# Kernel tuning notes

Measured on AMD Instinct MI355X. Metric: run time of the kernel, lower is better.

Reference implementation:

```python
import jax, jax.numpy as jnp
import numpy as np

B, N, C = 32, 16384, 256
D, H, S = 64, 128, 7
ITERS = 3
EPS = 1e-6
SCALE = D ** -0.5


def _ln(x, g, b):
    m = jnp.mean(x, axis=-1, keepdims=True)
    v = jnp.var(x, axis=-1, keepdims=True)
    return (x - m) / jnp.sqrt(v + 1e-5) * g + b


def _gru(x, h, Wih, Whh, bih, bhh):
    # PyTorch GRUCell: Wih/Whh are [3D, D]
    gi = x @ Wih.T + bih
    gh = h @ Whh.T + bhh
    ir, iz, inn = jnp.split(gi, 3, axis=-1)
    hr, hz, hn = jnp.split(gh, 3, axis=-1)
    r = jax.nn.sigmoid(ir + hr)
    z = jax.nn.sigmoid(iz + hz)
    n = jnp.tanh(inn + r * hn)
    return (1.0 - z) * n + z * h


def setup_inputs() -> dict:
    key = jax.random.key(0)
    ks = jax.random.split(key, 20)
    s_c = C ** -0.5
    s_d = D ** -0.5
    s_h = H ** -0.5
    p = {}
    p["inputs"] = jax.random.normal(ks[0], (B, N, C), jnp.float32)
    p["slots_mu"] = jax.random.normal(ks[1], (B, S, D), jnp.float32)
    p["ln_in_g"] = jnp.ones((C,), jnp.float32)
    p["ln_in_b"] = jnp.zeros((C,), jnp.float32)
    p["Wk"] = jax.random.normal(ks[2], (C, D), jnp.float32) * s_c
    p["Wv"] = jax.random.normal(ks[3], (C, D), jnp.float32) * s_c
    p["q_ln_g"] = jnp.ones((D,), jnp.float32)
    p["q_ln_b"] = jnp.zeros((D,), jnp.float32)
    p["Wq"] = jax.random.normal(ks[4], (D, D), jnp.float32) * s_d
    p["bq_ln_g"] = jnp.ones((D,), jnp.float32)
    p["bq_ln_b"] = jnp.zeros((D,), jnp.float32)
    p["bWq"] = jax.random.normal(ks[5], (D, D), jnp.float32) * s_d
    p["gru_Wih"] = jax.random.normal(ks[6], (3 * D, D), jnp.float32) * s_d
    p["gru_Whh"] = jax.random.normal(ks[7], (3 * D, D), jnp.float32) * s_d
    p["gru_bih"] = jnp.zeros((3 * D,), jnp.float32)
    p["gru_bhh"] = jnp.zeros((3 * D,), jnp.float32)
    p["mlp_ln_g"] = jnp.ones((D,), jnp.float32)
    p["mlp_ln_b"] = jnp.zeros((D,), jnp.float32)
    p["mlp_W1"] = jax.random.normal(ks[8], (D, H), jnp.float32) * s_d
    p["mlp_b1"] = jnp.zeros((H,), jnp.float32)
    p["mlp_W2"] = jax.random.normal(ks[9], (H, D), jnp.float32) * s_h
    p["mlp_b2"] = jnp.zeros((D,), jnp.float32)
    p["bmlp_ln_g"] = jnp.ones((D,), jnp.float32)
    p["bmlp_ln_b"] = jnp.zeros((D,), jnp.float32)
    p["bmlp_W1"] = jax.random.normal(ks[10], (D, H), jnp.float32) * s_d
    p["bmlp_b1"] = jnp.zeros((H,), jnp.float32)
    p["bmlp_W2"] = jax.random.normal(ks[11], (H, D), jnp.float32) * s_h
    p["bmlp_b2"] = jnp.zeros((D,), jnp.float32)
    return p


def reference(inputs, slots_mu, ln_in_g, ln_in_b, Wk, Wv, q_ln_g, q_ln_b, Wq,
              bq_ln_g, bq_ln_b, bWq, gru_Wih, gru_Whh, gru_bih, gru_bhh,
              mlp_ln_g, mlp_ln_b, mlp_W1, mlp_b1, mlp_W2, mlp_b2,
              bmlp_ln_g, bmlp_ln_b, bmlp_W1, bmlp_b1, bmlp_W2, bmlp_b2):
    x = _ln(inputs, ln_in_g, ln_in_b)          # [B,N,C]
    k = x @ Wk                                  # [B,N,D]
    v = x @ Wv                                  # [B,N,D]
    fg = slots_mu[:, :-1]                       # [B,S-1,D]
    bg = slots_mu[:, -1:]                       # [B,1,D]
    for _ in range(ITERS):
        fg_prev, bg_prev = fg, bg
        fq = _ln(fg, q_ln_g, q_ln_b) @ Wq
        bq = _ln(bg, bq_ln_g, bq_ln_b) @ bWq
        q = jnp.concatenate([fq, bq], axis=1)   # [B,S,D]
        logits = SCALE * jnp.einsum('bnd,bmd->bnm', k, q)  # [B,N,S]
        attn = jax.nn.softmax(logits, axis=-1) + EPS
        fa = attn[..., :-1]
        ba = attn[..., -1:]
        fa = fa / jnp.sum(fa, axis=1, keepdims=True)
        ba = ba / jnp.sum(ba, axis=1, keepdims=True)
        fu = jnp.einsum('bnm,bnd->bmd', fa, v)  # [B,S-1,D]
        bu = jnp.einsum('bnm,bnd->bmd', ba, v)  # [B,1,D]
        fg = _gru(fu.reshape(-1, D), fg_prev.reshape(-1, D),
                  gru_Wih, gru_Whh, gru_bih, gru_bhh).reshape(B, S - 1, D)
        fg = fg + (jax.nn.relu(_ln(fg, mlp_ln_g, mlp_ln_b) @ mlp_W1 + mlp_b1) @ mlp_W2 + mlp_b2)
        # NOTE: original code uses self.gru (shared) for bg, not bg_gru
        bg = _gru(bu.reshape(-1, D), bg_prev.reshape(-1, D),
                  gru_Wih, gru_Whh, gru_bih, gru_bhh).reshape(B, 1, D)
        bg = bg + (jax.nn.relu(_ln(bg, bmlp_ln_g, bmlp_ln_b) @ bmlp_W1 + bmlp_b1) @ bmlp_W2 + bmlp_b2)
    return jnp.concatenate([fg, bg], axis=1)    # [B,S,D]
```

## Files before the change

kernel.cpp:

```cpp
#include <hip/hip_runtime.h>
#include <hip/hip_bf16.h>

typedef __bf16 bf16_t;
typedef __bf16 bf16x4 __attribute__((ext_vector_type(4)));
typedef __bf16 bf16x8 __attribute__((ext_vector_type(8)));
typedef float f32x4 __attribute__((ext_vector_type(4)));

#define B_ 32
#define N_ 16384
#define C_ 256
#define D_ 64
#define ROWS_TOTAL (B_ * N_)

__device__ inline float wave_sum64(float v) {
#pragma unroll
  for (int o = 1; o < 64; o <<= 1) v += __shfl_xor(v, o);
  return v;
}

__device__ inline float sigmoidf_(float x) { return 1.0f / (1.0f + __expf(-x)); }
__device__ inline float tanhf_(float x) { return 1.0f - 2.0f / (__expf(2.0f * x) + 1.0f); }

__global__ __launch_bounds__(256) void prep_kernel(
    const float* __restrict__ Wk, const float* __restrict__ Wv,
    const float* __restrict__ Wih, const float* __restrict__ Whh,
    const float* __restrict__ slots, bf16_t* __restrict__ Wb,
    float* __restrict__ WihT, float* __restrict__ WhhT, float* __restrict__ g) {
  int i = blockIdx.x * 256 + threadIdx.x;
  if (i < 32768) {
    int j = i & 7, l = (i >> 3) & 63, t = (i >> 9) & 7, kb = i >> 12;
    int k = kb * 32 + (l >> 4) * 8 + j;
    int n = t * 16 + (l & 15);
    float v = (n < 64) ? Wk[k * 64 + n] : Wv[k * 64 + (n - 64)];
    Wb[i] = (bf16_t)v;
  } else if (i < 45056) {
    int idx = i - 32768;
    int c = idx / 192, j = idx % 192;
    WihT[idx] = Wih[j * 64 + c];
  } else if (i < 57344) {
    int idx = i - 45056;
    int c = idx / 192, j = idx % 192;
    WhhT[idx] = Whh[j * 64 + c];
  } else if (i < 71680) {
    int idx = i - 57344;
    g[idx] = slots[idx];
  }
}

__global__ __launch_bounds__(512) void proj_ln_kernel(
    const float* __restrict__ inp, const float* __restrict__ lng,
    const float* __restrict__ lnb, const bf16_t* __restrict__ Wb,
    bf16_t* __restrict__ kbuf, bf16_t* __restrict__ vbuf) {
  __shared__ bf16_t xs[128 * 256];
  const int tid = threadIdx.x, w = tid >> 6, lane = tid & 63;
  const int q4 = lane >> 4, lp = lane & 15;
  const long row0 = (long)blockIdx.x * 128;

  float4 gv[4], bv[4];
#pragma unroll
  for (int j = 0; j < 4; ++j) {
    gv[j] = *(const float4*)(lng + lp * 16 + j * 4);
    bv[j] = *(const float4*)(lnb + lp * 16 + j * 4);
  }

#pragma unroll
  for (int i = 0; i < 4; ++i) {
    int r = w * 16 + i * 4 + q4;
    const float* rp = inp + (row0 + r) * C_ + lp * 16;
    float4 x0 = *(const float4*)(rp);
    float4 x1 = *(const float4*)(rp + 4);
    float4 x2 = *(const float4*)(rp + 8);
    float4 x3 = *(const float4*)(rp + 12);
    float s = (x0.x + x0.y + x0.z + x0.w) + (x1.x + x1.y + x1.z + x1.w) +
              (x2.x + x2.y + x2.z + x2.w) + (x3.x + x3.y + x3.z + x3.w);
    float s2 = (x0.x * x0.x + x0.y * x0.y + x0.z * x0.z + x0.w * x0.w) +
               (x1.x * x1.x + x1.y * x1.y + x1.z * x1.z + x1.w * x1.w) +
               (x2.x * x2.x + x2.y * x2.y + x2.z * x2.z + x2.w * x2.w) +
               (x3.x * x3.x + x3.y * x3.y + x3.z * x3.z + x3.w * x3.w);
#pragma unroll
    for (int o = 1; o < 16; o <<= 1) {
      s += __shfl_xor(s, o);
      s2 += __shfl_xor(s2, o);
    }
    float mean = s * (1.0f / 256.0f);
    float var = s2 * (1.0f / 256.0f) - mean * mean;
    float rstd = rsqrtf(var + 1e-5f);
    bf16x8 y0, y1;
    y0[0] = (bf16_t)((x0.x - mean) * rstd * gv[0].x + bv[0].x);
    y0[1] = (bf16_t)((x0.y - mean) * rstd * gv[0].y + bv[0].y);
    y0[2] = (bf16_t)((x0.z - mean) * rstd * gv[0].z + bv[0].z);
    y0[3] = (bf16_t)((x0.w - mean) * rstd * gv[0].w + bv[0].w);
    y0[4] = (bf16_t)((x1.x - mean) * rstd * gv[1].x + bv[1].x);
    y0[5] = (bf16_t)((x1.y - mean) * rstd * gv[1].y + bv[1].y);
    y0[6] = (bf16_t)((x1.z - mean) * rstd * gv[1].z + bv[1].z);
    y0[7] = (bf16_t)((x1.w - mean) * rstd * gv[1].w + bv[1].w);
    y1[0] = (bf16_t)((x2.x - mean) * rstd * gv[2].x + bv[2].x);
    y1[1] = (bf16_t)((x2.y - mean) * rstd * gv[2].y + bv[2].y);
    y1[2] = (bf16_t)((x2.z - mean) * rstd * gv[2].z + bv[2].z);
    y1[3] = (bf16_t)((x2.w - mean) * rstd * gv[2].w + bv[2].w);
    y1[4] = (bf16_t)((x3.x - mean) * rstd * gv[3].x + bv[3].x);
    y1[5] = (bf16_t)((x3.y - mean) * rstd * gv[3].y + bv[3].y);
    y1[6] = (bf16_t)((x3.z - mean) * rstd * gv[3].z + bv[3].z);
    y1[7] = (bf16_t)((x3.w - mean) * rstd * gv[3].w + bv[3].w);
    int base = r * 32, swz = r & 31;
    *(bf16x8*)(xs + (size_t)(base + ((2 * lp) ^ swz)) * 8) = y0;
    *(bf16x8*)(xs + (size_t)(base + ((2 * lp + 1) ^ swz)) * 8) = y1;
  }
  __syncthreads();

  f32x4 acc[8];
  const f32x4 zf = {0.0f, 0.0f, 0.0f, 0.0f};
#pragma unroll
  for (int t = 0; t < 8; ++t) acc[t] = zf;

  const int r0 = w * 16 + lp;
  const int rsw = r0 & 31;
  for (int kb = 0; kb < 8; ++kb) {
    bf16x8 a = *(const bf16x8*)(xs + (size_t)(r0 * 32 + ((kb * 4 + q4) ^ rsw)) * 8);
#pragma unroll
    for (int t = 0; t < 8; ++t) {
      bf16x8 bfr = *(const bf16x8*)(Wb + (size_t)((kb * 8 + t) * 64 + lane) * 8);
      acc[t] = __builtin_amdgcn_mfma_f32_16x16x32_bf16(a, bfr, acc[t], 0, 0, 0);
    }
  }

#pragma unroll
  for (int t = 0; t < 8; ++t) {
    bf16_t* dst = (t < 4) ? kbuf : vbuf;
    int c = (t & 3) * 16 + lp;
#pragma unroll
    for (int reg = 0; reg < 4; ++reg) {
      long gr = row0 + w * 16 + q4 * 4 + reg;
      dst[gr * 64 + c] = (bf16_t)acc[t][reg];
    }
  }
}

__global__ __launch_bounds__(64) void qk_kernel(
    const float* __restrict__ g, const float* __restrict__ qg,
    const float* __restrict__ qb, const float* __restrict__ Wq,
    const float* __restrict__ bqg, const float* __restrict__ bqb,
    const float* __restrict__ bWq, float* __restrict__ q,
    float* __restrict__ acc, float* __restrict__ wsum) {
  __shared__ float sx[64];
  int bid = blockIdx.x, lane = threadIdx.x;
  int m = bid % 7;
  const float* lng = (m < 6) ? qg : bqg;
  const float* lnb = (m < 6) ? qb : bqb;
  const float* W = (m < 6) ? Wq : bWq;
  float gvv = g[bid * 64 + lane];
  float s = wave_sum64(gvv);
  float s2 = wave_sum64(gvv * gvv);
  float mean = s * (1.0f / 64.0f);
  float var = s2 * (1.0f / 64.0f) - mean * mean;
  float rstd = rsqrtf(var + 1e-5f);
  sx[lane] = (gvv - mean) * rstd * lng[lane] + lnb[lane];
  __syncthreads();
  float qd = 0.0f;
#pragma unroll 8
  for (int c = 0; c < 64; ++c) qd += sx[c] * W[c * 64 + lane];
  q[bid * 64 + lane] = qd;
  acc[bid * 64 + lane] = 0.0f;
  if (lane == 0) wsum[bid] = 0.0f;
}

__global__ __launch_bounds__(256) void attend_kernel(
    const bf16_t* __restrict__ kbuf, const bf16_t* __restrict__ vbuf,
    const float* __restrict__ q, float* __restrict__ acc,
    float* __restrict__ wsum) {
  __shared__ float qs[448];
  __shared__ float s_acc[448];
  __shared__ float s_w[7];
  int tid = threadIdx.x, w = tid >> 6, lane = tid & 63;
  int g4 = lane >> 4, lp = lane & 15;
  long chunk0 = (long)blockIdx.x * 512;
  int b = (int)(chunk0 >> 14);

  for (int idx = tid; idx < 448; idx += 256) {
    qs[idx] = q[b * 448 + idx];
    s_acc[idx] = 0.0f;
  }
  if (tid < 7) s_w[tid] = 0.0f;
  __syncthreads();

  float4 qv[7];
  const float4* qs4 = (const float4*)qs;
#pragma unroll
  for (int m = 0; m < 7; ++m) qv[m] = qs4[m * 16 + lp];

  float av[7][4];
  float wa[7];
#pragma unroll
  for (int m = 0; m < 7; ++m) {
    wa[m] = 0.0f;
#pragma unroll
    for (int j = 0; j < 4; ++j) av[m][j] = 0.0f;
  }

  for (int it = 0; it < 32; ++it) {
    long row = chunk0 + it * 16 + w * 4 + g4;
    bf16x4 kv = *(const bf16x4*)(kbuf + row * 64 + lp * 4);
    bf16x4 vv = *(const bf16x4*)(vbuf + row * 64 + lp * 4);
    float k0 = kv[0], k1 = kv[1], k2 = kv[2], k3 = kv[3];
    float lg[7];
#pragma unroll
    for (int m = 0; m < 7; ++m)
      lg[m] = k0 * qv[m].x + k1 * qv[m].y + k2 * qv[m].z + k3 * qv[m].w;
#pragma unroll
    for (int m = 0; m < 7; ++m) {
      lg[m] += __shfl_xor(lg[m], 1);
      lg[m] += __shfl_xor(lg[m], 2);
      lg[m] += __shfl_xor(lg[m], 4);
      lg[m] += __shfl_xor(lg[m], 8);
    }
    float mx = -1e30f;
#pragma unroll
    for (int m = 0; m < 7; ++m) {
      lg[m] *= 0.125f;
      mx = fmaxf(mx, lg[m]);
    }
    float e[7], s = 0.0f;
#pragma unroll
    for (int m = 0; m < 7; ++m) {
      e[m] = __expf(lg[m] - mx);
      s += e[m];
    }
    float inv = 1.0f / s;
    float v0 = vv[0], v1 = vv[1], v2 = vv[2], v3 = vv[3];
#pragma unroll
    for (int m = 0; m < 7; ++m) {
      float a = e[m] * inv + 1e-6f;
      wa[m] += a;
      av[m][0] += a * v0;
      av[m][1] += a * v1;
      av[m][2] += a * v2;
      av[m][3] += a * v3;
    }
  }

#pragma unroll
  for (int m = 0; m < 7; ++m) {
#pragma unroll
    for (int j = 0; j < 4; ++j) {
      av[m][j] += __shfl_xor(av[m][j], 16);
      av[m][j] += __shfl_xor(av[m][j], 32);
    }
    wa[m] += __shfl_xor(wa[m], 16);
    wa[m] += __shfl_xor(wa[m], 32);
  }
  if (g4 == 0) {
#pragma unroll
    for (int m = 0; m < 7; ++m)
#pragma unroll
      for (int j = 0; j < 4; ++j) atomicAdd(&s_acc[m * 64 + lp * 4 + j], av[m][j]);
  }
  if (lane == 0) {
#pragma unroll
    for (int m = 0; m < 7; ++m) atomicAdd(&s_w[m], wa[m]);
  }
  __syncthreads();
  for (int idx = tid; idx < 448; idx += 256) atomicAdd(&acc[b * 448 + idx], s_acc[idx]);
  if (tid < 7) atomicAdd(&wsum[b * 7 + tid], s_w[tid]);
}

__global__ __launch_bounds__(192) void update_kernel(
    const float* __restrict__ acc, const float* __restrict__ wsum,
    const float* __restrict__ g, const float* __restrict__ WihT,
    const float* __restrict__ WhhT, const float* __restrict__ bih,
    const float* __restrict__ bhh, const float* __restrict__ mlg,
    const float* __restrict__ mlb, const float* __restrict__ mW1,
    const float* __restrict__ mb1, const float* __restrict__ mW2,
    const float* __restrict__ mb2, const float* __restrict__ bmlg,
    const float* __restrict__ bmlb, const float* __restrict__ bW1,
    const float* __restrict__ bb1, const float* __restrict__ bW2,
    const float* __restrict__ bb2, float* __restrict__ gout,
    const float* __restrict__ qg, const float* __restrict__ qb,
    const float* __restrict__ Wq, const float* __restrict__ bqg,
    const float* __restrict__ bqb, const float* __restrict__ bWq,
    float* __restrict__ qout, float* __restrict__ accz,
    float* __restrict__ wsz, int write_q) {
  __shared__ float fu[64], hp[64], gi[192], gh[192], h2[64], xb[64], a1[128], go[64];
  int tid = threadIdx.x, bid = blockIdx.x, m = bid % 7;

  const float *lg_, *lb_, *W1_, *b1_, *W2_, *b2_;
  if (m < 6) { lg_ = mlg; lb_ = mlb; W1_ = mW1; b1_ = mb1; W2_ = mW2; b2_ = mb2; }
  else       { lg_ = bmlg; lb_ = bmlb; W1_ = bW1; b1_ = bb1; W2_ = bW2; b2_ = bb2; }

  if (tid < 64) {
    float wv = wsum[bid];
    fu[tid] = acc[bid * 64 + tid] / wv;
    hp[tid] = g[bid * 64 + tid];
  }
  __syncthreads();

  {
    int j = tid;
    float a = bih[j], bsum = bhh[j];
    for (int c = 0; c < 64; ++c) {
      a += fu[c] * WihT[c * 192 + j];
      bsum += hp[c] * WhhT[c * 192 + j];
    }
    gi[j] = a;
    gh[j] = bsum;
  }
  __syncthreads();

  if (tid < 64) {
    int d = tid;
    float r = sigmoidf_(gi[d] + gh[d]);
    float z = sigmoidf_(gi[64 + d] + gh[64 + d]);
    float n = tanhf_(gi[128 + d] + r * gh[128 + d]);
    float h = (1.0f - z) * n + z * hp[d];
    h2[d] = h;
    float s = wave_sum64(h);
    float s2 = wave_sum64(h * h);
    float mean = s * (1.0f / 64.0f);
    float var = s2 * (1.0f / 64.0f) - mean * mean;
    xb[d] = (h - mean) * rsqrtf(var + 1e-5f) * lg_[d] + lb_[d];
  }
  __syncthreads();

  if (tid < 128) {
    int hh = tid;
    float a = b1_[hh];
    for (int c = 0; c < 64; ++c) a += xb[c] * W1_[c * 128 + hh];
    a1[hh] = fmaxf(a, 0.0f);
  }
  __syncthreads();

  if (tid < 64) {
    int d = tid;
    float o = b2_[d];
    for (int hh = 0; hh < 128; ++hh) o += a1[hh] * W2_[hh * 64 + d];
    float res = h2[d] + o;
    gout[bid * 64 + d] = res;
    go[d] = res;
  }
  __syncthreads();

  if (write_q) {
    if (tid < 64) {
      const float* qlng = (m < 6) ? qg : bqg;
      const float* qlnb = (m < 6) ? qb : bqb;
      const float* W = (m < 6) ? Wq : bWq;
      float gvv = go[tid];
      float s = wave_sum64(gvv);
      float s2 = wave_sum64(gvv * gvv);
      float mean = s * (1.0f / 64.0f);
      float var = s2 * (1.0f / 64.0f) - mean * mean;
      xb[tid] = (gvv - mean) * rsqrtf(var + 1e-5f) * qlng[tid] + qlnb[tid];
      __syncwarp();
      float qd = 0.0f;
      const float* Wl = W;
#pragma unroll 8
      for (int c = 0; c < 64; ++c) qd += xb[c] * Wl[c * 64 + tid];
      qout[bid * 64 + tid] = qd;
      accz[bid * 64 + tid] = 0.0f;
      if (tid == 0) wsz[bid] = 0.0f;
    }
  }
}

extern "C" void kernel_launch(void* const* d_in, const int* in_sizes, int n_in,
                              void* d_out, int out_size, void* d_ws, size_t ws_size,
                              hipStream_t stream) {
  const float* inputs   = (const float*)d_in[0];
  const float* slots_mu = (const float*)d_in[1];
  const float* ln_in_g  = (const float*)d_in[2];
  const float* ln_in_b  = (const float*)d_in[3];
  const float* Wk       = (const float*)d_in[4];
  const float* Wv       = (const float*)d_in[5];
  const float* q_ln_g   = (const float*)d_in[6];
  const float* q_ln_b   = (const float*)d_in[7];
  const float* Wq       = (const float*)d_in[8];
  const float* bq_ln_g  = (const float*)d_in[9];
  const float* bq_ln_b  = (const float*)d_in[10];
  const float* bWq      = (const float*)d_in[11];
  const float* gru_Wih  = (const float*)d_in[12];
  const float* gru_Whh  = (const float*)d_in[13];
  const float* gru_bih  = (const float*)d_in[14];
  const float* gru_bhh  = (const float*)d_in[15];
  const float* mlp_ln_g = (const float*)d_in[16];
  const float* mlp_ln_b = (const float*)d_in[17];
  const float* mlp_W1   = (const float*)d_in[18];
  const float* mlp_b1   = (const float*)d_in[19];
  const float* mlp_W2   = (const float*)d_in[20];
  const float* mlp_b2   = (const float*)d_in[21];
  const float* bmlp_ln_g = (const float*)d_in[22];
  const float* bmlp_ln_b = (const float*)d_in[23];
  const float* bmlp_W1  = (const float*)d_in[24];
  const float* bmlp_b1  = (const float*)d_in[25];
  const float* bmlp_W2  = (const float*)d_in[26];
  const float* bmlp_b2  = (const float*)d_in[27];
  float* out = (float*)d_out;

  char* ws = (char*)d_ws;
  const size_t KV_BYTES = (size_t)ROWS_TOTAL * 64 * 2;
  bf16_t* kbuf = (bf16_t*)ws;
  bf16_t* vbuf = (bf16_t*)(ws + KV_BYTES);
  bf16_t* Wb   = (bf16_t*)(ws + 2 * KV_BYTES);
  float* WihT  = (float*)(ws + 2 * KV_BYTES + 65536);
  float* WhhT  = (float*)(ws + 2 * KV_BYTES + 65536 + 49152);
  float* gbuf  = (float*)(ws + 2 * KV_BYTES + 65536 + 2 * 49152);
  float* qbuf  = (float*)(ws + 2 * KV_BYTES + 65536 + 2 * 49152 + 57344);
  float* accb  = (float*)(ws + 2 * KV_BYTES + 65536 + 2 * 49152 + 2 * 57344);
  float* wsumb = (float*)(ws + 2 * KV_BYTES + 65536 + 2 * 49152 + 3 * 57344);

  prep_kernel<<<280, 256, 0, stream>>>(Wk, Wv, gru_Wih, gru_Whh, slots_mu, Wb,
                                       WihT, WhhT, gbuf);
  proj_ln_kernel<<<ROWS_TOTAL / 128, 512, 0, stream>>>(inputs, ln_in_g, ln_in_b,
                                                       Wb, kbuf, vbuf);
  qk_kernel<<<224, 64, 0, stream>>>(gbuf, q_ln_g, q_ln_b, Wq, bq_ln_g, bq_ln_b,
                                    bWq, qbuf, accb, wsumb);
  for (int it = 0; it < 3; ++it) {
    attend_kernel<<<ROWS_TOTAL / 512, 256, 0, stream>>>(kbuf, vbuf, qbuf, accb,
                                                        wsumb);
    update_kernel<<<224, 192, 0, stream>>>(
        accb, wsumb, gbuf, WihT, WhhT, gru_bih, gru_bhh, mlp_ln_g, mlp_ln_b,
        mlp_W1, mlp_b1, mlp_W2, mlp_b2, bmlp_ln_g, bmlp_ln_b, bmlp_W1, bmlp_b1,
        bmlp_W2, bmlp_b2, (it == 2) ? out : gbuf, q_ln_g, q_ln_b, Wq, bq_ln_g,
        bq_ln_b, bWq, qbuf, accb, wsumb, (it < 2) ? 1 : 0);
  }
}
```

Before: 1.035 ms.

## Fuse first-iteration attention into the K/V projection kernel epilogue

Moves the query computation before the projection and computes the first iteration's softmax attention and weighted value accumulation directly from the projection's accumulators. This removes one full attend pass that re-reads the K/V buffers from memory. It adds register pressure and extra ALU work to the projection kernel, and the first iteration now uses fp32 rather than bf16-rounded K/V.

```diff
diff --git a/kernel.cpp b/kernel.cpp
--- a/kernel.cpp
+++ b/kernel.cpp
@@ -47,14 +47,54 @@
   }
 }
 
+__global__ __launch_bounds__(64) void qk_kernel(
+    const float* __restrict__ g, const float* __restrict__ qg,
+    const float* __restrict__ qb, const float* __restrict__ Wq,
+    const float* __restrict__ bqg, const float* __restrict__ bqb,
+    const float* __restrict__ bWq, float* __restrict__ q,
+    float* __restrict__ acc, float* __restrict__ wsum) {
+  __shared__ float sx[64];
+  int bid = blockIdx.x, lane = threadIdx.x;
+  int m = bid % 7;
+  const float* lng = (m < 6) ? qg : bqg;
+  const float* lnb = (m < 6) ? qb : bqb;
+  const float* W = (m < 6) ? Wq : bWq;
+  float gvv = g[bid * 64 + lane];
+  float s = wave_sum64(gvv);
+  float s2 = wave_sum64(gvv * gvv);
+  float mean = s * (1.0f / 64.0f);
+  float var = s2 * (1.0f / 64.0f) - mean * mean;
+  float rstd = rsqrtf(var + 1e-5f);
+  sx[lane] = (gvv - mean) * rstd * lng[lane] + lnb[lane];
+  __syncthreads();
+  float qd = 0.0f;
+#pragma unroll 8
+  for (int c = 0; c < 64; ++c) qd += sx[c] * W[c * 64 + lane];
+  q[bid * 64 + lane] = qd;
+  acc[bid * 64 + lane] = 0.0f;
+  if (lane == 0) wsum[bid] = 0.0f;
+}
+
 __global__ __launch_bounds__(512) void proj_ln_kernel(
     const float* __restrict__ inp, const float* __restrict__ lng,
     const float* __restrict__ lnb, const bf16_t* __restrict__ Wb,
-    bf16_t* __restrict__ kbuf, bf16_t* __restrict__ vbuf) {
+    bf16_t* __restrict__ kbuf, bf16_t* __restrict__ vbuf,
+    const float* __restrict__ q, float* __restrict__ acc_g,
+    float* __restrict__ wsum_g) {
   __shared__ bf16_t xs[128 * 256];
+  __shared__ float qs[448];
+  __shared__ float s_acc[448];
+  __shared__ float s_w[7];
   const int tid = threadIdx.x, w = tid >> 6, lane = tid & 63;
   const int q4 = lane >> 4, lp = lane & 15;
   const long row0 = (long)blockIdx.x * 128;
+  const int b = (int)(row0 >> 14);
+
+  for (int idx = tid; idx < 448; idx += 512) {
+    qs[idx] = q[b * 448 + idx];
+    s_acc[idx] = 0.0f;
+  }
+  if (tid < 7) s_w[tid] = 0.0f;
 
   float4 gv[4], bv[4];
 #pragma unroll
@@ -134,34 +174,81 @@
       dst[gr * 64 + c] = (bf16_t)acc[t][reg];
     }
   }
-}
-
-__global__ __launch_bounds__(64) void qk_kernel(
-    const float* __restrict__ g, const float* __restrict__ qg,
-    const float* __restrict__ qb, const float* __restrict__ Wq,
-    const float* __restrict__ bqg, const float* __restrict__ bqb,
-    const float* __restrict__ bWq, float* __restrict__ q,
-    float* __restrict__ acc, float* __restrict__ wsum) {
-  __shared__ float sx[64];
-  int bid = blockIdx.x, lane = threadIdx.x;
-  int m = bid % 7;
-  const float* lng = (m < 6) ? qg : bqg;
-  const float* lnb = (m < 6) ? qb : bqb;
-  const float* W = (m < 6) ? Wq : bWq;
-  float gvv = g[bid * 64 + lane];
-  float s = wave_sum64(gvv);
-  float s2 = wave_sum64(gvv * gvv);
-  float mean = s * (1.0f / 64.0f);
-  float var = s2 * (1.0f / 64.0f) - mean * mean;
-  float rstd = rsqrtf(var + 1e-5f);
-  sx[lane] = (gvv - mean) * rstd * lng[lane] + lnb[lane];
-  __syncthreads();
-  float qd = 0.0f;
-#pragma unroll 8
-  for (int c = 0; c < 64; ++c) qd += sx[c] * W[c * 64 + lane];
-  q[bid * 64 + lane] = qd;
-  acc[bid * 64 + lane] = 0.0f;
-  if (lane == 0) wsum[bid] = 0.0f;
+
+  float av[7][4];
+  float wa[7];
+#pragma unroll
+  for (int m = 0; m < 7; ++m) {
+    wa[m] = 0.0f;
+#pragma unroll
+    for (int t = 0; t < 4; ++t) av[m][t] = 0.0f;
+  }
+
+#pragma unroll
+  for (int reg = 0; reg < 4; ++reg) {
+    float p[7];
+#pragma unroll
+    for (int m = 0; m < 7; ++m) p[m] = 0.0f;
+#pragma unroll
+    for (int t = 0; t < 4; ++t) {
+      float at = acc[t][reg];
+#pragma unroll
+      for (int m = 0; m < 7; ++m) p[m] += at * qs[m * 64 + t * 16 + lp];
+    }
+#pragma unroll
+    for (int m = 0; m < 7; ++m) {
+      p[m] += __shfl_xor(p[m], 1);
+      p[m] += __shfl_xor(p[m], 2);
+      p[m] += __shfl_xor(p[m], 4);
+      p[m] += __shfl_xor(p[m], 8);
+    }
+    float mx = -1e30f;
+#pragma unroll
+    for (int m = 0; m < 7; ++m) {
+      p[m] *= 0.125f;
+      mx = fmaxf(mx, p[m]);
+    }
+    float s = 0.0f;
+#pragma unroll
+    for (int m = 0; m < 7; ++m) {
+      p[m] = __expf(p[m] - mx);
+      s += p[m];
+    }
+    float inv = 1.0f / s;
+#pragma unroll
+    for (int m = 0; m < 7; ++m) {
+      float a = p[m] * inv + 1e-6f;
+      wa[m] += a;
+#pragma unroll
+      for (int t = 0; t < 4; ++t) av[m][t] += a * acc[4 + t][reg];
+    }
+  }
+
+#pragma unroll
+  for (int m = 0; m < 7; ++m) {
+#pragma unroll
+    for (int t = 0; t < 4; ++t) {
+      av[m][t] += __shfl_xor(av[m][t], 16);
+      av[m][t] += __shfl_xor(av[m][t], 32);
+    }
+    wa[m] += __shfl_xor(wa[m], 16);
+    wa[m] += __shfl_xor(wa[m], 32);
+  }
+  if (q4 == 0) {
+#pragma unroll
+    for (int m = 0; m < 7; ++m)
+#pragma unroll
+      for (int t = 0; t < 4; ++t)
+        atomicAdd(&s_acc[m * 64 + t * 16 + lp], av[m][t]);
+  }
+  if (lane == 0) {
+#pragma unroll
+    for (int m = 0; m < 7; ++m) atomicAdd(&s_w[m], wa[m]);
+  }
+  __syncthreads();
+  for (int idx = tid; idx < 448; idx += 512)
+    atomicAdd(&acc_g[b * 448 + idx], s_acc[idx]);
+  if (tid < 7) atomicAdd(&wsum_g[b * 7 + tid], s_w[tid]);
 }
 
 __global__ __launch_bounds__(256) void attend_kernel(
@@ -408,13 +495,14 @@
 
   prep_kernel<<<280, 256, 0, stream>>>(Wk, Wv, gru_Wih, gru_Whh, slots_mu, Wb,
                                        WihT, WhhT, gbuf);
-  proj_ln_kernel<<<ROWS_TOTAL / 128, 512, 0, stream>>>(inputs, ln_in_g, ln_in_b,
-                                                       Wb, kbuf, vbuf);
   qk_kernel<<<224, 64, 0, stream>>>(gbuf, q_ln_g, q_ln_b, Wq, bq_ln_g, bq_ln_b,
                                     bWq, qbuf, accb, wsumb);
+  proj_ln_kernel<<<ROWS_TOTAL / 128, 512, 0, stream>>>(
+      inputs, ln_in_g, ln_in_b, Wb, kbuf, vbuf, qbuf, accb, wsumb);
   for (int it = 0; it < 3; ++it) {
-    attend_kernel<<<ROWS_TOTAL / 512, 256, 0, stream>>>(kbuf, vbuf, qbuf, accb,
-                                                        wsumb);
+    if (it > 0)
+      attend_kernel<<<ROWS_TOTAL / 512, 256, 0, stream>>>(kbuf, vbuf, qbuf,
+                                                          accb, wsumb);
     update_kernel<<<224, 192, 0, stream>>>(
         accb, wsumb, gbuf, WihT, WhhT, gru_bih, gru_bhh, mlp_ln_g, mlp_ln_b,
         mlp_W1, mlp_b1, mlp_W2, mlp_b2, bmlp_ln_g, bmlp_ln_b, bmlp_W1, bmlp_b1,
```

Result: slower. 1.059 ms (+2.3%).
